# Kernel optimization log

Hardware: AMD Instinct MI355X
Metric: run time of the kernel (lower is better)

Reference implementation:

```python
import jax, jax.numpy as jnp
import numpy as np

B, L, D, H, M, DFF = 16, 2048, 512, 8, 64, 2048
E = D // H
KERNELS = (13, 25)
K = len(KERNELS)


def _moving_avg(x, k):
    # Autoformer-style moving average: replicate-pad (k-1)//2 at both ends, AvgPool1d stride 1.
    pad = (k - 1) // 2
    xp = jnp.concatenate([jnp.repeat(x[:, :1], pad, axis=1), x, jnp.repeat(x[:, -1:], pad, axis=1)], axis=1)
    cs = jnp.cumsum(xp, axis=1)
    cs = jnp.concatenate([jnp.zeros_like(cs[:, :1]), cs], axis=1)
    return (cs[:, k:] - cs[:, :-k]) / k  # [B, L, D] for odd k


def _decomp(x, w, b):
    # mixture-of-experts decomposition: softmax(Linear(1->K)(x)) weighted sum of K moving averages
    means = jnp.stack([_moving_avg(x, k) for k in KERNELS], axis=-1)  # [B,L,D,K]
    gate = jax.nn.softmax(x[..., None] * w + b, axis=-1)              # [B,L,D,K]
    mean = jnp.sum(means * gate, axis=-1)
    return x - mean


def _forward(x, Wq, bq, Wk, bk, Wv, bv, Wo, bo, four_wr, four_wi, conv1_w, conv2_w, dec1_w, dec1_b, dec2_w, dec2_b, mode_index):
    Bx, Lx, Dx = x.shape
    # q/k/v projections (FourierBlock only consumes q; k,v projected per AutoCorrelationLayer)
    q = x @ Wq.T + bq
    _ = x @ Wk.T + bk
    _ = x @ Wv.T + bv
    qh = q.reshape(Bx, Lx, H, E).transpose(0, 2, 3, 1)  # [B,H,E,L]
    x_ft = jnp.fft.rfft(qh, axis=-1)                     # [B,H,E,L//2+1]
    xsel = x_ft[..., mode_index]                         # [B,H,E,M] gather selected modes
    w = (four_wr + 1j * four_wi).astype(x_ft.dtype)      # [H,E,E,M]
    out = jnp.einsum('bhem,heom->bhom', xsel, w)         # per-mode complex channel mix
    out_ft = jnp.zeros((Bx, H, E, Lx // 2 + 1), x_ft.dtype).at[..., :M].set(out)
    y = jnp.fft.irfft(out_ft, n=Lx, axis=-1)             # [B,H,E,L]
    y = y.transpose(0, 3, 1, 2).reshape(Bx, Lx, Dx)      # mix=True: seq-major before merge
    u = x + (y @ Wo.T + bo)
    r1 = _decomp(u, dec1_w, dec1_b)
    ffn = jax.nn.gelu(r1 @ conv1_w.T, approximate=False) @ conv2_w.T  # 1x1 convs == pointwise linears
    return _decomp(r1 + ffn, dec2_w, dec2_b)


def setup_inputs() -> dict:
    key = jax.random.key(0)
    ks = jax.random.split(key, 16)
    s = 0.02
    rng = np.random.default_rng(0)
    mode_index = jnp.asarray(np.sort(rng.choice(L // 2, size=M, replace=False)).astype(np.int32))
    scale = 1.0 / (D * D)
    return {
        'x': jax.random.normal(ks[0], (B, L, D), jnp.float32),
        'Wq': s * jax.random.normal(ks[1], (D, D), jnp.float32),
        'bq': jnp.zeros((D,), jnp.float32),
        'Wk': s * jax.random.normal(ks[2], (D, D), jnp.float32),
        'bk': jnp.zeros((D,), jnp.float32),
        'Wv': s * jax.random.normal(ks[3], (D, D), jnp.float32),
        'bv': jnp.zeros((D,), jnp.float32),
        'Wo': s * jax.random.normal(ks[4], (D, D), jnp.float32),
        'bo': jnp.zeros((D,), jnp.float32),
        'four_wr': scale * jax.random.uniform(ks[5], (H, E, E, M), jnp.float32),
        'four_wi': scale * jax.random.uniform(ks[6], (H, E, E, M), jnp.float32),
        'conv1_w': s * jax.random.normal(ks[7], (DFF, D), jnp.float32),
        'conv2_w': s * jax.random.normal(ks[8], (D, DFF), jnp.float32),
        'dec1_w': 0.1 * jax.random.normal(ks[9], (K,), jnp.float32),
        'dec1_b': jnp.zeros((K,), jnp.float32),
        'dec2_w': 0.1 * jax.random.normal(ks[10], (K,), jnp.float32),
        'dec2_b': jnp.zeros((K,), jnp.float32),
        'mode_index': mode_index,
    }


def reference(x, Wq, bq, Wk, bk, Wv, bv, Wo, bo, four_wr, four_wi, conv1_w, conv2_w, dec1_w, dec1_b, dec2_w, dec2_b, mode_index):
    return _forward(x, Wq, bq, Wk, bk, Wv, bv, Wo, bo, four_wr, four_wi, conv1_w, conv2_w, dec1_w, dec1_b, dec2_w, dec2_b, mode_index)
```

## Files before the change

### kernel.cpp

```cpp
#include <hip/hip_runtime.h>
#include <math.h>


#define EPI_GELU   1
#define EPI_RES    2
#define EPI_SPLIT  3
#define EPI_WQFOLD 4
#define EPI_INVU   5

typedef __attribute__((ext_vector_type(8))) short short8;
typedef __attribute__((ext_vector_type(4))) float f32x4;

#define AS1 __attribute__((address_space(1)))
#define AS3 __attribute__((address_space(3)))

__device__ __forceinline__ void gll16(const void* g, void* l) {
    __builtin_amdgcn_global_load_lds((const AS1 void*)g, (AS3 void*)l, 16, 0, 0);
}

__device__ __forceinline__ float gelu_exact(float v) {
    return 0.5f * v * (1.0f + erff(v * 0.70710678118654752f));
}

__device__ __forceinline__ unsigned short f2bf(float f) {
    unsigned u = __builtin_bit_cast(unsigned, f);
    unsigned r = (u + 0x7fffu + ((u >> 16) & 1u)) >> 16;
    return (unsigned short)r;
}
__device__ __forceinline__ float bf2f(unsigned short h) {
    unsigned u = ((unsigned)h) << 16;
    return __builtin_bit_cast(float, u);
}

template<int BM, int BN, int EPI, bool ALO, bool BLO>
__global__ __launch_bounds__(512)
void gemm_hl(const unsigned short* __restrict__ Ah, const unsigned short* __restrict__ Al, long long sAb,
             const unsigned short* __restrict__ Bh, const unsigned short* __restrict__ Bl, long long sBb,
             float* __restrict__ Cf, unsigned short* __restrict__ Ch, unsigned short* __restrict__ Cl,
             long long sCb,
             const unsigned short* __restrict__ Rh, const unsigned short* __restrict__ Rl,
             const float* __restrict__ resf, long long sRb,
             const float* __restrict__ bias, const int* __restrict__ midx,
             int N, int K)
{
    constexpr int MI = BM / 32, NJ = BN / 64;
    __shared__ __align__(16) unsigned short sA[ALO ? 2 : 1][BM * 32];
    __shared__ __align__(16) unsigned short sB[BLO ? 2 : 1][BN * 32];

    const int tid = threadIdx.x, lane = tid & 63, wid = tid >> 6;
    const int wm = wid >> 2, wn = wid & 3;
    const int m0 = blockIdx.y * BM, n0 = blockIdx.x * BN;
    const int z = blockIdx.z;

    Ah += (size_t)z * sAb; if (ALO) Al += (size_t)z * sAb;
    Bh += (size_t)z * sBb; if (BLO) Bl += (size_t)z * sBb;

    f32x4 acc[MI][NJ] = {};

    const int srr = lane >> 2;
    const int sp  = lane & 3;

    for (int k0 = 0; k0 < K; k0 += 32) {
        for (int ch = wid; ch < BM / 16; ch += 8) {
            int row = ch * 16 + srr;
            int ls = sp ^ ((row >> 1) & 3);
            size_t g = (size_t)(m0 + row) * K + k0 + ls * 8;
            gll16(Ah + g, &sA[0][ch * 512]);
            if (ALO) gll16(Al + g, &sA[1][ch * 512]);
        }
        for (int ch = wid; ch < BN / 16; ch += 8) {
            int row = ch * 16 + srr;
            int ls = sp ^ ((row >> 1) & 3);
            size_t g = (size_t)(n0 + row) * K + k0 + ls * 8;
            gll16(Bh + g, &sB[0][ch * 512]);
            if (BLO) gll16(Bl + g, &sB[1][ch * 512]);
        }
        __syncthreads();

        short8 a[ALO ? 2 : 1][MI], b[BLO ? 2 : 1][NJ];
        const int s = lane >> 4;
#pragma unroll
        for (int i = 0; i < MI; ++i) {
            int r = wm * (BM / 2) + i * 16 + (lane & 15);
            int off = r * 32 + (s ^ ((r >> 1) & 3)) * 8;
            a[0][i] = *reinterpret_cast<const short8*>(&sA[0][off]);
            if (ALO) a[1][i] = *reinterpret_cast<const short8*>(&sA[1][off]);
        }
#pragma unroll
        for (int j = 0; j < NJ; ++j) {
            int r = wn * (BN / 4) + j * 16 + (lane & 15);
            int off = r * 32 + (s ^ ((r >> 1) & 3)) * 8;
            b[0][j] = *reinterpret_cast<const short8*>(&sB[0][off]);
            if (BLO) b[1][j] = *reinterpret_cast<const short8*>(&sB[1][off]);
        }
#pragma unroll
        for (int i = 0; i < MI; ++i)
#pragma unroll
            for (int j = 0; j < NJ; ++j) {
                acc[i][j] = __builtin_amdgcn_mfma_f32_16x16x32_bf16(a[0][i], b[0][j], acc[i][j], 0, 0, 0);
                if (BLO)
                    acc[i][j] = __builtin_amdgcn_mfma_f32_16x16x32_bf16(a[0][i], b[1][j], acc[i][j], 0, 0, 0);
                if (ALO)
                    acc[i][j] = __builtin_amdgcn_mfma_f32_16x16x32_bf16(a[1][i], b[0][j], acc[i][j], 0, 0, 0);
            }
        __syncthreads();
    }

    const int cr = (lane >> 4) * 4, cc = lane & 15;
#pragma unroll
    for (int i = 0; i < MI; ++i)
#pragma unroll
        for (int j = 0; j < NJ; ++j)
#pragma unroll
            for (int r = 0; r < 4; ++r) {
                int m = m0 + wm * (BM / 2) + i * 16 + cr + r;
                int n = n0 + wn * (BN / 4) + j * 16 + cc;
                size_t idx = (size_t)z * sCb + (size_t)m * N + n;
                float v = acc[i][j][r];
                if (EPI == EPI_GELU) {
                    Ch[idx] = f2bf(gelu_exact(v));
                } else if (EPI == EPI_RES) {
                    size_t ri = (size_t)m * N + n;
                    Cf[idx] = v + bf2f(Rh[ri]) + bf2f(Rl[ri]);
                } else if (EPI == EPI_SPLIT) {
                    unsigned short h = f2bf(v);
                    Ch[idx] = h;
                    Cl[idx] = f2bf(v - bf2f(h));
                } else if (EPI == EPI_WQFOLD) {
                    if (n < 64 && midx[n] == 0) v += bias[m] * 2048.0f;
                    Cf[idx] = v;
                } else if (EPI == EPI_INVU) {
                    size_t ri = (size_t)z * sRb + (size_t)m * N + n;
                    Cf[idx] = v + resf[ri] + bias[n];
                }
            }
}

__global__ __launch_bounds__(256)
void gemm_dft(const unsigned short* __restrict__ Ath, const unsigned short* __restrict__ Atl,
              const float* __restrict__ X, long long sXb,
              float* __restrict__ P)
{
    __shared__ __align__(16) unsigned short sA[2][64 * 32];
    __shared__ __align__(16) unsigned sB[2][64 * 20];

    const int tid = threadIdx.x, lane = tid & 63, wid = tid >> 6;
    const int wm = wid >> 1, wn = wid & 1;
    const int m0 = blockIdx.y * 64, n0 = blockIdx.x * 64;
    const int z = blockIdx.z;
    const int b = z >> 2, ks = z & 3;
    X += (size_t)b * sXb;

    f32x4 acc[2][2] = {};

    const int arow = wid * 16 + (lane >> 2);
    const int als  = (lane & 3) ^ ((arow >> 1) & 3);
    const int lp = tid >> 4;
    const int d4 = (tid & 15) * 4;

    for (int kk = 0; kk < 512; kk += 32) {
        const int k0 = ks * 512 + kk;
        size_t gA = (size_t)(m0 + arow) * 2048 + k0 + als * 8;
        gll16(Ath + gA, &sA[0][wid * 512]);
        gll16(Atl + gA, &sA[1][wid * 512]);

        const float* xr = &X[(size_t)(k0 + 2 * lp) * 512 + n0 + d4];
        float4 v0 = *reinterpret_cast<const float4*>(xr);
        float4 v1 = *reinterpret_cast<const float4*>(xr + 512);
        float a0[4] = {v0.x, v0.y, v0.z, v0.w};
        float a1[4] = {v1.x, v1.y, v1.z, v1.w};
#pragma unroll
        for (int i = 0; i < 4; ++i) {
            int row = d4 + i;
            int slot = lp ^ (((row >> 3) & 3) << 2);
            unsigned short h0 = f2bf(a0[i]), h1 = f2bf(a1[i]);
            sB[0][row * 20 + slot] = (unsigned)h0 | ((unsigned)h1 << 16);
            unsigned short l0 = f2bf(a0[i] - bf2f(h0)), l1 = f2bf(a1[i] - bf2f(h1));
            sB[1][row * 20 + slot] = (unsigned)l0 | ((unsigned)l1 << 16);
        }
        __syncthreads();

        short8 a[2][2], b2[2][2];
        const int s = lane >> 4;
#pragma unroll
        for (int i = 0; i < 2; ++i) {
            int r = wm * 32 + i * 16 + (lane & 15);
            int off = r * 32 + (s ^ ((r >> 1) & 3)) * 8;
            a[0][i] = *reinterpret_cast<const short8*>(&sA[0][off]);
            a[1][i] = *reinterpret_cast<const short8*>(&sA[1][off]);
        }
#pragma unroll
        for (int j = 0; j < 2; ++j) {
            int d = wn * 32 + j * 16 + (lane & 15);
            int off = d * 20 + ((s * 4) ^ (((d >> 3) & 3) << 2));
            b2[0][j] = *reinterpret_cast<const short8*>(&sB[0][off]);
            b2[1][j] = *reinterpret_cast<const short8*>(&sB[1][off]);
        }
#pragma unroll
        for (int i = 0; i < 2; ++i)
#pragma unroll
            for (int j = 0; j < 2; ++j) {
                acc[i][j] = __builtin_amdgcn_mfma_f32_16x16x32_bf16(a[0][i], b2[0][j], acc[i][j], 0, 0, 0);
                acc[i][j] = __builtin_amdgcn_mfma_f32_16x16x32_bf16(a[0][i], b2[1][j], acc[i][j], 0, 0, 0);
                acc[i][j] = __builtin_amdgcn_mfma_f32_16x16x32_bf16(a[1][i], b2[0][j], acc[i][j], 0, 0, 0);
            }
        __syncthreads();
    }

    const int cr = (lane >> 4) * 4, cc = lane & 15;
#pragma unroll
    for (int i = 0; i < 2; ++i)
#pragma unroll
        for (int j = 0; j < 2; ++j)
#pragma unroll
            for (int r = 0; r < 4; ++r) {
                int m = m0 + wm * 32 + i * 16 + cr + r;
                int n = n0 + wn * 32 + j * 16 + cc;
                P[((size_t)z * 128 + m) * 512 + n] = acc[i][j][r];
            }
}

__global__ __launch_bounds__(256)
void dft_reduce(const float* __restrict__ P, unsigned short* __restrict__ Oh,
                unsigned short* __restrict__ Ol)
{
    int i = blockIdx.x * 256 + threadIdx.x;
    int b = i >> 14;
    int r = i & 16383;
    const float4* p = reinterpret_cast<const float4*>(P) + ((size_t)b * 4) * 16384 + r;
    float4 v = p[0];
    float4 v1 = p[16384], v2 = p[2 * 16384], v3 = p[3 * 16384];
    v.x += v1.x + v2.x + v3.x;
    v.y += v1.y + v2.y + v3.y;
    v.z += v1.z + v2.z + v3.z;
    v.w += v1.w + v2.w + v3.w;
    ushort4 h, l;
    h.x = f2bf(v.x); l.x = f2bf(v.x - bf2f(h.x));
    h.y = f2bf(v.y); l.y = f2bf(v.y - bf2f(h.y));
    h.z = f2bf(v.z); l.z = f2bf(v.z - bf2f(h.z));
    h.w = f2bf(v.w); l.w = f2bf(v.w - bf2f(h.w));
    size_t o = (size_t)b * 16384 + r;
    reinterpret_cast<ushort4*>(Oh)[o] = h;
    reinterpret_cast<ushort4*>(Ol)[o] = l;
}

__global__ __launch_bounds__(256)
void split_f32_kernel(const float* __restrict__ src, unsigned short* __restrict__ hi,
                      unsigned short* __restrict__ lo, int n4)
{
    int i = blockIdx.x * 256 + threadIdx.x;
    if (i >= n4) return;
    float4 v = reinterpret_cast<const float4*>(src)[i];
    ushort4 h, l;
    h.x = f2bf(v.x); l.x = f2bf(v.x - bf2f(h.x));
    h.y = f2bf(v.y); l.y = f2bf(v.y - bf2f(h.y));
    h.z = f2bf(v.z); l.z = f2bf(v.z - bf2f(h.z));
    h.w = f2bf(v.w); l.w = f2bf(v.w - bf2f(h.w));
    reinterpret_cast<ushort4*>(hi)[i] = h;
    reinterpret_cast<ushort4*>(lo)[i] = l;
}

__global__ void build_tables_kernel(const int* __restrict__ midx,
                                    unsigned short* __restrict__ fth, unsigned short* __restrict__ ftl,
                                    unsigned short* __restrict__ ith, unsigned short* __restrict__ itl)
{
    const int l = blockIdx.x;
    const int t = threadIdx.x;
    const int m = t & 63;
    const bool im = t >= 64;
    const float c0 = 6.28318530717958647692f / 2048.0f;

    int f = midx[m];
    int ph = (f * l) & 2047;
    float s, c;
    sincosf(c0 * (float)ph, &s, &c);
    float v = im ? -s : c;
    unsigned short h = f2bf(v);
    fth[(size_t)t * 2048 + l] = h;
    ftl[(size_t)t * 2048 + l] = f2bf(v - bf2f(h));

    int ph2 = (m * l) & 2047;
    float s2, c2;
    sincosf(c0 * (float)ph2, &s2, &c2);
    float v2 = im ? s2 : c2;
    unsigned short h2 = f2bf(v2);
    ith[(size_t)l * 128 + t] = h2;
    itl[(size_t)l * 128 + t] = f2bf(v2 - bf2f(h2));
}

__global__ __launch_bounds__(256)
void mode_mix_kernel(const float* __restrict__ xsel,
                     const float* __restrict__ wr, const float* __restrict__ wi,
                     unsigned short* __restrict__ cth, unsigned short* __restrict__ ctl)
{
    const int m = blockIdx.x;
    const int h = blockIdx.y;
    const int tid = threadIdx.x;

    __shared__ float xr[16][64], xi[16][64];
    __shared__ float wrs[64][65], wis[64][65];

    for (int i = tid; i < 4096; i += 256) {
        int e = i >> 6, o = i & 63;
        size_t g = (((size_t)h * 64 + e) * 64 + o) * 64 + m;
        wrs[e][o] = wr[g];
        wis[e][o] = wi[g];
    }
    for (int i = tid; i < 1024; i += 256) {
        int bb = i >> 6, e = i & 63;
        size_t g = ((size_t)bb * 512 + h * 64 + e) * 128;
        xr[bb][e] = xsel[g + m];
        xi[bb][e] = xsel[g + 64 + m];
    }
    __syncthreads();

    const int o = tid & 63;
    const int bq4 = tid >> 6;
    const float sc_r = (m == 0) ? (1.0f / 2048.0f) : (2.0f / 2048.0f);
    const float sc_i = (m == 0) ? 0.0f : (-2.0f / 2048.0f);

    for (int q = 0; q < 4; ++q) {
        int bb = bq4 * 4 + q;
        float or_ = 0.f, oi_ = 0.f;
#pragma unroll 16
        for (int e = 0; e < 64; ++e) {
            float xrv = xr[bb][e], xiv = xi[bb][e];
            float wrv = wrs[e][o], wiv = wis[e][o];
            or_ += xrv * wrv - xiv * wiv;
            oi_ += xrv * wiv + xiv * wrv;
        }
        size_t base = ((size_t)bb * 128 + m) * 512 + (size_t)h * 64 + o;
        float vr = or_ * sc_r;
        unsigned short hr = f2bf(vr);
        cth[base] = hr; ctl[base] = f2bf(vr - bf2f(hr));
        float vi = oi_ * sc_i;
        unsigned short hi2 = f2bf(vi);
        cth[base + 64 * 512] = hi2; ctl[base + 64 * 512] = f2bf(vi - bf2f(hi2));
    }
}

template<bool SPLIT>
__global__ __launch_bounds__(256)
void decomp_kernel(const float* __restrict__ X, float* __restrict__ Rf,
                   unsigned short* __restrict__ Rh, unsigned short* __restrict__ Rl,
                   const float* __restrict__ w, const float* __restrict__ bg)
{
    const int d = blockIdx.x * 256 + threadIdx.x;
    const int l0 = blockIdx.y * 64;
    const int b = blockIdx.z;
    const float w0 = w[0], w1 = w[1], b0 = bg[0], b1 = bg[1];

    const float* Xp = X + (size_t)b * 2048 * 512 + d;
    const size_t obase = (size_t)b * 2048 * 512 + d;

    float s1 = 0.f, s2 = 0.f;
    for (int i = l0 - 12; i <= l0 + 12; ++i) {
        int ic = min(max(i, 0), 2047);
        float v = Xp[(size_t)ic * 512];
        s2 += v;
        if (i >= l0 - 6 && i <= l0 + 6) s1 += v;
    }
    for (int l = l0; l < l0 + 64; ++l) {
        float xv = Xp[(size_t)l * 512];
        float m1 = s1 * (1.0f / 13.0f);
        float m2 = s2 * (1.0f / 25.0f);
        float e0 = xv * w0 + b0, e1 = xv * w1 + b1;
        float mx = fmaxf(e0, e1);
        float g0 = expf(e0 - mx), g1 = expf(e1 - mx);
        float mean = (g0 * m1 + g1 * m2) / (g0 + g1);
        float rv = xv - mean;
        size_t oi = obase + (size_t)l * 512;
        if (SPLIT) {
            unsigned short h = f2bf(rv);
            Rh[oi] = h;
            Rl[oi] = f2bf(rv - bf2f(h));
        } else {
            Rf[oi] = rv;
        }
        s1 += Xp[(size_t)min(l + 7, 2047) * 512] - Xp[(size_t)max(l - 6, 0) * 512];
        s2 += Xp[(size_t)min(l + 13, 2047) * 512] - Xp[(size_t)max(l - 12, 0) * 512];
    }
}

extern "C" void kernel_launch(void* const* d_in, const int* in_sizes, int n_in,
                              void* d_out, int out_size, void* d_ws, size_t ws_size,
                              hipStream_t stream)
{
    const float* x    = (const float*)d_in[0];
    const float* Wq   = (const float*)d_in[1];
    const float* bq   = (const float*)d_in[2];
    const float* Wo   = (const float*)d_in[7];
    const float* bo   = (const float*)d_in[8];
    const float* fwr  = (const float*)d_in[9];
    const float* fwi  = (const float*)d_in[10];
    const float* c1w  = (const float*)d_in[11];
    const float* c2w  = (const float*)d_in[12];
    const float* d1w  = (const float*)d_in[13];
    const float* d1b  = (const float*)d_in[14];
    const float* d2w  = (const float*)d_in[15];
    const float* d2b  = (const float*)d_in[16];
    const int*   midx = (const int*)d_in[17];
    float* out = (float*)d_out;
    float* ws  = (float*)d_ws;

    float* region0 = ws;
    unsigned short* p1 = (unsigned short*)(ws + 16777216);
    unsigned short* fth = p1;
    unsigned short* ftl = p1 + 262144;
    unsigned short* ith = p1 + 2 * 262144;
    unsigned short* itl = p1 + 3 * 262144;
    unsigned short* wqh = p1 + 4 * 262144;
    unsigned short* wql = p1 + 5 * 262144;
    unsigned short* woh = p1 + 6 * 262144;
    unsigned short* wol = p1 + 7 * 262144;
    unsigned short* xfh = p1 + 2097152;
    unsigned short* xfl = p1 + 3145728;
    unsigned short* cth = p1 + 4194304;
    unsigned short* ctl = p1 + 5242880;
    unsigned short* zth = p1 + 6291456;
    unsigned short* ztl = p1 + 7340288;
    float* xsel = (float*)(p1 + 8388608);

    unsigned short* c1h = p1;
    unsigned short* c1l = p1 + 1048576;
    unsigned short* c2h = p1 + 2 * 1048576;
    unsigned short* c2l = p1 + 3 * 1048576;
    unsigned short* hh  = (unsigned short*)(ws + 18874368);
    const size_t hbase = 72ull << 20;
    const int R = (ws_size >= hbase + (size_t)8192 * 2048 * 2) ? 8192 : 4096;

    unsigned short* r1h = (unsigned short*)d_out;
    unsigned short* r1l = r1h + 16777216;

    const long long sBL = (long long)2048 * 512;
    const long long sP  = 65536;

    build_tables_kernel<<<2048, 128, 0, stream>>>(midx, fth, ftl, ith, itl);
    split_f32_kernel<<<256, 256, 0, stream>>>(Wq, wqh, wql, 65536);
    split_f32_kernel<<<256, 256, 0, stream>>>(Wo, woh, wol, 65536);

    gemm_dft<<<dim3(8, 2, 64), 256, 0, stream>>>(fth, ftl, x, sBL, region0);
    dft_reduce<<<1024, 256, 0, stream>>>(region0, xfh, xfl);

    gemm_hl<64, 64, EPI_WQFOLD, true, true><<<dim3(2, 8, 16), 512, 0, stream>>>(
        wqh, wql, 0, xfh, xfl, sP, xsel, nullptr, nullptr, sP,
        nullptr, nullptr, nullptr, 0, bq, midx, 128, 512);

    mode_mix_kernel<<<dim3(64, 8), 256, 0, stream>>>(xsel, fwr, fwi, cth, ctl);

    gemm_hl<64, 64, EPI_SPLIT, true, true><<<dim3(2, 8, 16), 512, 0, stream>>>(
        woh, wol, 0, cth, ctl, sP, nullptr, zth, ztl, sP,
        nullptr, nullptr, nullptr, 0, nullptr, nullptr, 128, 512);

    gemm_hl<128, 64, EPI_INVU, true, true><<<dim3(8, 16, 16), 512, 0, stream>>>(
        ith, itl, 0, zth, ztl, sP, region0, nullptr, nullptr, sBL,
        nullptr, nullptr, x, sBL, bo, nullptr, 512, 128);

    decomp_kernel<true><<<dim3(2, 32, 16), 256, 0, stream>>>(
        region0, nullptr, r1h, r1l, d1w, d1b);

    split_f32_kernel<<<1024, 256, 0, stream>>>(c1w, c1h, c1l, 262144);
    split_f32_kernel<<<1024, 256, 0, stream>>>(c2w, c2h, c2l, 262144);

    const int nc = 32768 / R;
    for (int c = 0; c < nc; ++c) {
        const unsigned short* r1hc = r1h + (size_t)c * R * 512;
        const unsigned short* r1lc = r1l + (size_t)c * R * 512;
        gemm_hl<128, 128, EPI_GELU, true, true><<<dim3(16, R / 128), 512, 0, stream>>>(
            r1hc, r1lc, 0, c1h, c1l, 0, nullptr, hh, nullptr, 0,
            nullptr, nullptr, nullptr, 0, nullptr, nullptr, 2048, 512);
        gemm_hl<128, 64, EPI_RES, false, true><<<dim3(8, R / 128), 512, 0, stream>>>(
            hh, nullptr, 0, c2h, c2l, 0, region0 + (size_t)c * R * 512, nullptr, nullptr, 0,
            r1hc, r1lc, nullptr, 0, nullptr, nullptr, 512, 2048);
    }

    decomp_kernel<false><<<dim3(2, 32, 16), 256, 0, stream>>>(
        region0, out, nullptr, nullptr, d2w, d2b);
}
```

Before: 840.3 us.

## Drop hi/lo bf16 split, use single bf16 GEMMs with XCD-aware block swizzle

```diff
diff --git a/kernel.cpp b/kernel.cpp
--- a/kernel.cpp
+++ b/kernel.cpp
@@ -4,7 +4,7 @@
 
 #define EPI_GELU   1
 #define EPI_RES    2
-#define EPI_SPLIT  3
+#define EPI_BF16   3
 #define EPI_WQFOLD 4
 #define EPI_INVU   5
 
@@ -32,28 +32,35 @@
     return __builtin_bit_cast(float, u);
 }
 
-template<int BM, int BN, int EPI, bool ALO, bool BLO>
+template<int BM, int BN, int EPI>
 __global__ __launch_bounds__(512)
-void gemm_hl(const unsigned short* __restrict__ Ah, const unsigned short* __restrict__ Al, long long sAb,
-             const unsigned short* __restrict__ Bh, const unsigned short* __restrict__ Bl, long long sBb,
-             float* __restrict__ Cf, unsigned short* __restrict__ Ch, unsigned short* __restrict__ Cl,
-             long long sCb,
+void gemm_hl(const unsigned short* __restrict__ Ah, long long sAb,
+             const unsigned short* __restrict__ Bh, long long sBb,
+             float* __restrict__ Cf, unsigned short* __restrict__ Ch, long long sCb,
              const unsigned short* __restrict__ Rh, const unsigned short* __restrict__ Rl,
              const float* __restrict__ resf, long long sRb,
              const float* __restrict__ bias, const int* __restrict__ midx,
              int N, int K)
 {
     constexpr int MI = BM / 32, NJ = BN / 64;
-    __shared__ __align__(16) unsigned short sA[ALO ? 2 : 1][BM * 32];
-    __shared__ __align__(16) unsigned short sB[BLO ? 2 : 1][BN * 32];
+    __shared__ __align__(16) unsigned short sA[BM * 32];
+    __shared__ __align__(16) unsigned short sB[BN * 32];
 
     const int tid = threadIdx.x, lane = tid & 63, wid = tid >> 6;
     const int wm = wid >> 2, wn = wid & 3;
-    const int m0 = blockIdx.y * BM, n0 = blockIdx.x * BN;
+
+    const int gx = gridDim.x;
+    int flat = blockIdx.y * gx + blockIdx.x;
+    const int nwg = gx * gridDim.y;
+    if ((nwg & 7) == 0) {
+        const int cpx = nwg >> 3;
+        flat = (flat & 7) * cpx + (flat >> 3);
+    }
+    const int m0 = (flat / gx) * BM, n0 = (flat % gx) * BN;
     const int z = blockIdx.z;
 
-    Ah += (size_t)z * sAb; if (ALO) Al += (size_t)z * sAb;
-    Bh += (size_t)z * sBb; if (BLO) Bl += (size_t)z * sBb;
+    Ah += (size_t)z * sAb;
+    Bh += (size_t)z * sBb;
 
     f32x4 acc[MI][NJ] = {};
 
@@ -64,45 +71,32 @@
         for (int ch = wid; ch < BM / 16; ch += 8) {
             int row = ch * 16 + srr;
             int ls = sp ^ ((row >> 1) & 3);
-            size_t g = (size_t)(m0 + row) * K + k0 + ls * 8;
-            gll16(Ah + g, &sA[0][ch * 512]);
-            if (ALO) gll16(Al + g, &sA[1][ch * 512]);
+            gll16(Ah + (size_t)(m0 + row) * K + k0 + ls * 8, &sA[ch * 512]);
         }
         for (int ch = wid; ch < BN / 16; ch += 8) {
             int row = ch * 16 + srr;
             int ls = sp ^ ((row >> 1) & 3);
-            size_t g = (size_t)(n0 + row) * K + k0 + ls * 8;
-            gll16(Bh + g, &sB[0][ch * 512]);
-            if (BLO) gll16(Bl + g, &sB[1][ch * 512]);
+            gll16(Bh + (size_t)(n0 + row) * K + k0 + ls * 8, &sB[ch * 512]);
         }
         __syncthreads();
 
-        short8 a[ALO ? 2 : 1][MI], b[BLO ? 2 : 1][NJ];
+        short8 a[MI], b[NJ];
         const int s = lane >> 4;
 #pragma unroll
         for (int i = 0; i < MI; ++i) {
             int r = wm * (BM / 2) + i * 16 + (lane & 15);
-            int off = r * 32 + (s ^ ((r >> 1) & 3)) * 8;
-            a[0][i] = *reinterpret_cast<const short8*>(&sA[0][off]);
-            if (ALO) a[1][i] = *reinterpret_cast<const short8*>(&sA[1][off]);
+            a[i] = *reinterpret_cast<const short8*>(&sA[r * 32 + (s ^ ((r >> 1) & 3)) * 8]);
         }
 #pragma unroll
         for (int j = 0; j < NJ; ++j) {
             int r = wn * (BN / 4) + j * 16 + (lane & 15);
-            int off = r * 32 + (s ^ ((r >> 1) & 3)) * 8;
-            b[0][j] = *reinterpret_cast<const short8*>(&sB[0][off]);
-            if (BLO) b[1][j] = *reinterpret_cast<const short8*>(&sB[1][off]);
+            b[j] = *reinterpret_cast<const short8*>(&sB[r * 32 + (s ^ ((r >> 1) & 3)) * 8]);
         }
 #pragma unroll
         for (int i = 0; i < MI; ++i)
 #pragma unroll
-            for (int j = 0; j < NJ; ++j) {
-                acc[i][j] = __builtin_amdgcn_mfma_f32_16x16x32_bf16(a[0][i], b[0][j], acc[i][j], 0, 0, 0);
-                if (BLO)
-                    acc[i][j] = __builtin_amdgcn_mfma_f32_16x16x32_bf16(a[0][i], b[1][j], acc[i][j], 0, 0, 0);
-                if (ALO)
-                    acc[i][j] = __builtin_amdgcn_mfma_f32_16x16x32_bf16(a[1][i], b[0][j], acc[i][j], 0, 0, 0);
-            }
+            for (int j = 0; j < NJ; ++j)
+                acc[i][j] = __builtin_amdgcn_mfma_f32_16x16x32_bf16(a[i], b[j], acc[i][j], 0, 0, 0);
         __syncthreads();
     }
 
@@ -122,10 +116,8 @@
                 } else if (EPI == EPI_RES) {
                     size_t ri = (size_t)m * N + n;
                     Cf[idx] = v + bf2f(Rh[ri]) + bf2f(Rl[ri]);
-                } else if (EPI == EPI_SPLIT) {
-                    unsigned short h = f2bf(v);
-                    Ch[idx] = h;
-                    Cl[idx] = f2bf(v - bf2f(h));
+                } else if (EPI == EPI_BF16) {
+                    Ch[idx] = f2bf(v);
                 } else if (EPI == EPI_WQFOLD) {
                     if (n < 64 && midx[n] == 0) v += bias[m] * 2048.0f;
                     Cf[idx] = v;
@@ -137,12 +129,12 @@
 }
 
 __global__ __launch_bounds__(256)
-void gemm_dft(const unsigned short* __restrict__ Ath, const unsigned short* __restrict__ Atl,
+void gemm_dft(const unsigned short* __restrict__ Ath,
               const float* __restrict__ X, long long sXb,
               float* __restrict__ P)
 {
-    __shared__ __align__(16) unsigned short sA[2][64 * 32];
-    __shared__ __align__(16) unsigned sB[2][64 * 20];
+    __shared__ __align__(16) unsigned short sA[64 * 32];
+    __shared__ __align__(16) unsigned sB[64 * 20];
 
     const int tid = threadIdx.x, lane = tid & 63, wid = tid >> 6;
     const int wm = wid >> 1, wn = wid & 1;
@@ -160,9 +152,7 @@
 
     for (int kk = 0; kk < 512; kk += 32) {
         const int k0 = ks * 512 + kk;
-        size_t gA = (size_t)(m0 + arow) * 2048 + k0 + als * 8;
-        gll16(Ath + gA, &sA[0][wid * 512]);
-        gll16(Atl + gA, &sA[1][wid * 512]);
+        gll16(Ath + (size_t)(m0 + arow) * 2048 + k0 + als * 8, &sA[wid * 512]);
 
         const float* xr = &X[(size_t)(k0 + 2 * lp) * 512 + n0 + d4];
         float4 v0 = *reinterpret_cast<const float4*>(xr);
@@ -173,37 +163,28 @@
         for (int i = 0; i < 4; ++i) {
             int row = d4 + i;
             int slot = lp ^ (((row >> 3) & 3) << 2);
-            unsigned short h0 = f2bf(a0[i]), h1 = f2bf(a1[i]);
-            sB[0][row * 20 + slot] = (unsigned)h0 | ((unsigned)h1 << 16);
-            unsigned short l0 = f2bf(a0[i] - bf2f(h0)), l1 = f2bf(a1[i] - bf2f(h1));
-            sB[1][row * 20 + slot] = (unsigned)l0 | ((unsigned)l1 << 16);
+            sB[row * 20 + slot] = (unsigned)f2bf(a0[i]) | ((unsigned)f2bf(a1[i]) << 16);
         }
         __syncthreads();
 
-        short8 a[2][2], b2[2][2];
+        short8 a[2], b2[2];
         const int s = lane >> 4;
 #pragma unroll
         for (int i = 0; i < 2; ++i) {
             int r = wm * 32 + i * 16 + (lane & 15);
-            int off = r * 32 + (s ^ ((r >> 1) & 3)) * 8;
-            a[0][i] = *reinterpret_cast<const short8*>(&sA[0][off]);
-            a[1][i] = *reinterpret_cast<const short8*>(&sA[1][off]);
+            a[i] = *reinterpret_cast<const short8*>(&sA[r * 32 + (s ^ ((r >> 1) & 3)) * 8]);
         }
 #pragma unroll
         for (int j = 0; j < 2; ++j) {
             int d = wn * 32 + j * 16 + (lane & 15);
             int off = d * 20 + ((s * 4) ^ (((d >> 3) & 3) << 2));
-            b2[0][j] = *reinterpret_cast<const short8*>(&sB[0][off]);
-            b2[1][j] = *reinterpret_cast<const short8*>(&sB[1][off]);
+            b2[j] = *reinterpret_cast<const short8*>(&sB[off]);
         }
 #pragma unroll
         for (int i = 0; i < 2; ++i)
 #pragma unroll
-            for (int j = 0; j < 2; ++j) {
-                acc[i][j] = __builtin_amdgcn_mfma_f32_16x16x32_bf16(a[0][i], b2[0][j], acc[i][j], 0, 0, 0);
-                acc[i][j] = __builtin_amdgcn_mfma_f32_16x16x32_bf16(a[0][i], b2[1][j], acc[i][j], 0, 0, 0);
-                acc[i][j] = __builtin_amdgcn_mfma_f32_16x16x32_bf16(a[1][i], b2[0][j], acc[i][j], 0, 0, 0);
-            }
+            for (int j = 0; j < 2; ++j)
+                acc[i][j] = __builtin_amdgcn_mfma_f32_16x16x32_bf16(a[i], b2[j], acc[i][j], 0, 0, 0);
         __syncthreads();
     }
 
@@ -221,8 +202,7 @@
 }
 
 __global__ __launch_bounds__(256)
-void dft_reduce(const float* __restrict__ P, unsigned short* __restrict__ Oh,
-                unsigned short* __restrict__ Ol)
+void dft_reduce(const float* __restrict__ P, unsigned short* __restrict__ Oh)
 {
     int i = blockIdx.x * 256 + threadIdx.x;
     int b = i >> 14;
@@ -234,35 +214,25 @@
     v.y += v1.y + v2.y + v3.y;
     v.z += v1.z + v2.z + v3.z;
     v.w += v1.w + v2.w + v3.w;
-    ushort4 h, l;
-    h.x = f2bf(v.x); l.x = f2bf(v.x - bf2f(h.x));
-    h.y = f2bf(v.y); l.y = f2bf(v.y - bf2f(h.y));
-    h.z = f2bf(v.z); l.z = f2bf(v.z - bf2f(h.z));
-    h.w = f2bf(v.w); l.w = f2bf(v.w - bf2f(h.w));
-    size_t o = (size_t)b * 16384 + r;
-    reinterpret_cast<ushort4*>(Oh)[o] = h;
-    reinterpret_cast<ushort4*>(Ol)[o] = l;
+    ushort4 h;
+    h.x = f2bf(v.x); h.y = f2bf(v.y); h.z = f2bf(v.z); h.w = f2bf(v.w);
+    reinterpret_cast<ushort4*>(Oh)[(size_t)b * 16384 + r] = h;
 }
 
 __global__ __launch_bounds__(256)
-void split_f32_kernel(const float* __restrict__ src, unsigned short* __restrict__ hi,
-                      unsigned short* __restrict__ lo, int n4)
+void cvt_bf16_kernel(const float* __restrict__ src, unsigned short* __restrict__ hi, int n4)
 {
     int i = blockIdx.x * 256 + threadIdx.x;
     if (i >= n4) return;
     float4 v = reinterpret_cast<const float4*>(src)[i];
-    ushort4 h, l;
-    h.x = f2bf(v.x); l.x = f2bf(v.x - bf2f(h.x));
-    h.y = f2bf(v.y); l.y = f2bf(v.y - bf2f(h.y));
-    h.z = f2bf(v.z); l.z = f2bf(v.z - bf2f(h.z));
-    h.w = f2bf(v.w); l.w = f2bf(v.w - bf2f(h.w));
+    ushort4 h;
+    h.x = f2bf(v.x); h.y = f2bf(v.y); h.z = f2bf(v.z); h.w = f2bf(v.w);
     reinterpret_cast<ushort4*>(hi)[i] = h;
-    reinterpret_cast<ushort4*>(lo)[i] = l;
 }
 
 __global__ void build_tables_kernel(const int* __restrict__ midx,
-                                    unsigned short* __restrict__ fth, unsigned short* __restrict__ ftl,
-                                    unsigned short* __restrict__ ith, unsigned short* __restrict__ itl)
+                                    unsigned short* __restrict__ fth,
+                                    unsigned short* __restrict__ ith)
 {
     const int l = blockIdx.x;
     const int t = threadIdx.x;
@@ -274,24 +244,18 @@
     int ph = (f * l) & 2047;
     float s, c;
     sincosf(c0 * (float)ph, &s, &c);
-    float v = im ? -s : c;
-    unsigned short h = f2bf(v);
-    fth[(size_t)t * 2048 + l] = h;
-    ftl[(size_t)t * 2048 + l] = f2bf(v - bf2f(h));
+    fth[(size_t)t * 2048 + l] = f2bf(im ? -s : c);
 
     int ph2 = (m * l) & 2047;
     float s2, c2;
     sincosf(c0 * (float)ph2, &s2, &c2);
-    float v2 = im ? s2 : c2;
-    unsigned short h2 = f2bf(v2);
-    ith[(size_t)l * 128 + t] = h2;
-    itl[(size_t)l * 128 + t] = f2bf(v2 - bf2f(h2));
+    ith[(size_t)l * 128 + t] = f2bf(im ? s2 : c2);
 }
 
 __global__ __launch_bounds__(256)
 void mode_mix_kernel(const float* __restrict__ xsel,
                      const float* __restrict__ wr, const float* __restrict__ wi,
-                     unsigned short* __restrict__ cth, unsigned short* __restrict__ ctl)
+                     unsigned short* __restrict__ cth)
 {
     const int m = blockIdx.x;
     const int h = blockIdx.y;
@@ -330,12 +294,8 @@
             oi_ += xrv * wiv + xiv * wrv;
         }
         size_t base = ((size_t)bb * 128 + m) * 512 + (size_t)h * 64 + o;
-        float vr = or_ * sc_r;
-        unsigned short hr = f2bf(vr);
-        cth[base] = hr; ctl[base] = f2bf(vr - bf2f(hr));
-        float vi = oi_ * sc_i;
-        unsigned short hi2 = f2bf(vi);
-        cth[base + 64 * 512] = hi2; ctl[base + 64 * 512] = f2bf(vi - bf2f(hi2));
+        cth[base] = f2bf(or_ * sc_r);
+        cth[base + 64 * 512] = f2bf(oi_ * sc_i);
     }
 }
 
@@ -346,7 +306,7 @@
                    const float* __restrict__ w, const float* __restrict__ bg)
 {
     const int d = blockIdx.x * 256 + threadIdx.x;
-    const int l0 = blockIdx.y * 64;
+    const int l0 = blockIdx.y * 32;
     const int b = blockIdx.z;
     const float w0 = w[0], w1 = w[1], b0 = bg[0], b1 = bg[1];
 
@@ -360,7 +320,7 @@
         s2 += v;
         if (i >= l0 - 6 && i <= l0 + 6) s1 += v;
     }
-    for (int l = l0; l < l0 + 64; ++l) {
+    for (int l = l0; l < l0 + 32; ++l) {
         float xv = Xp[(size_t)l * 512];
         float m1 = s1 * (1.0f / 13.0f);
         float m2 = s2 * (1.0f / 25.0f);
@@ -406,25 +366,16 @@
     float* region0 = ws;
     unsigned short* p1 = (unsigned short*)(ws + 16777216);
     unsigned short* fth = p1;
-    unsigned short* ftl = p1 + 262144;
-    unsigned short* ith = p1 + 2 * 262144;
-    unsigned short* itl = p1 + 3 * 262144;
-    unsigned short* wqh = p1 + 4 * 262144;
-    unsigned short* wql = p1 + 5 * 262144;
-    unsigned short* woh = p1 + 6 * 262144;
-    unsigned short* wol = p1 + 7 * 262144;
-    unsigned short* xfh = p1 + 2097152;
-    unsigned short* xfl = p1 + 3145728;
-    unsigned short* cth = p1 + 4194304;
-    unsigned short* ctl = p1 + 5242880;
-    unsigned short* zth = p1 + 6291456;
-    unsigned short* ztl = p1 + 7340288;
-    float* xsel = (float*)(p1 + 8388608);
+    unsigned short* ith = p1 + 262144;
+    unsigned short* wqh = p1 + 2 * 262144;
+    unsigned short* woh = p1 + 3 * 262144;
+    unsigned short* xfh = p1 + 1048576;
+    unsigned short* cth = p1 + 2097152;
+    unsigned short* zth = p1 + 3145728;
+    float* xsel = (float*)(p1 + 4194304);
 
     unsigned short* c1h = p1;
-    unsigned short* c1l = p1 + 1048576;
-    unsigned short* c2h = p1 + 2 * 1048576;
-    unsigned short* c2l = p1 + 3 * 1048576;
+    unsigned short* c2h = p1 + 1048576;
     unsigned short* hh  = (unsigned short*)(ws + 18874368);
     const size_t hbase = 72ull << 20;
     const int R = (ws_size >= hbase + (size_t)8192 * 2048 * 2) ? 8192 : 4096;
@@ -435,45 +386,45 @@
     const long long sBL = (long long)2048 * 512;
     const long long sP  = 65536;
 
-    build_tables_kernel<<<2048, 128, 0, stream>>>(midx, fth, ftl, ith, itl);
-    split_f32_kernel<<<256, 256, 0, stream>>>(Wq, wqh, wql, 65536);
-    split_f32_kernel<<<256, 256, 0, stream>>>(Wo, woh, wol, 65536);
-
-    gemm_dft<<<dim3(8, 2, 64), 256, 0, stream>>>(fth, ftl, x, sBL, region0);
-    dft_reduce<<<1024, 256, 0, stream>>>(region0, xfh, xfl);
-
-    gemm_hl<64, 64, EPI_WQFOLD, true, true><<<dim3(2, 8, 16), 512, 0, stream>>>(
-        wqh, wql, 0, xfh, xfl, sP, xsel, nullptr, nullptr, sP,
+    build_tables_kernel<<<2048, 128, 0, stream>>>(midx, fth, ith);
+    cvt_bf16_kernel<<<256, 256, 0, stream>>>(Wq, wqh, 65536);
+    cvt_bf16_kernel<<<256, 256, 0, stream>>>(Wo, woh, 65536);
+
+    gemm_dft<<<dim3(8, 2, 64), 256, 0, stream>>>(fth, x, sBL, region0);
+    dft_reduce<<<1024, 256, 0, stream>>>(region0, xfh);
+
+    gemm_hl<64, 64, EPI_WQFOLD><<<dim3(2, 8, 16), 512, 0, stream>>>(
+        wqh, 0, xfh, sP, xsel, nullptr, sP,
         nullptr, nullptr, nullptr, 0, bq, midx, 128, 512);
 
-    mode_mix_kernel<<<dim3(64, 8), 256, 0, stream>>>(xsel, fwr, fwi, cth, ctl);
-
-    gemm_hl<64, 64, EPI_SPLIT, true, true><<<dim3(2, 8, 16), 512, 0, stream>>>(
-        woh, wol, 0, cth, ctl, sP, nullptr, zth, ztl, sP,
+    mode_mix_kernel<<<dim3(64, 8), 256, 0, stream>>>(xsel, fwr, fwi, cth);
+
+    gemm_hl<64, 64, EPI_BF16><<<dim3(2, 8, 16), 512, 0, stream>>>(
+        woh, 0, cth, sP, nullptr, zth, sP,
         nullptr, nullptr, nullptr, 0, nullptr, nullptr, 128, 512);
 
-    gemm_hl<128, 64, EPI_INVU, true, true><<<dim3(8, 16, 16), 512, 0, stream>>>(
-        ith, itl, 0, zth, ztl, sP, region0, nullptr, nullptr, sBL,
+    gemm_hl<128, 128, EPI_INVU><<<dim3(4, 16, 16), 512, 0, stream>>>(
+        ith, 0, zth, sP, region0, nullptr, sBL,
         nullptr, nullptr, x, sBL, bo, nullptr, 512, 128);
 
-    decomp_kernel<true><<<dim3(2, 32, 16), 256, 0, stream>>>(
+    decomp_kernel<true><<<dim3(2, 64, 16), 256, 0, stream>>>(
         region0, nullptr, r1h, r1l, d1w, d1b);
 
-    split_f32_kernel<<<1024, 256, 0, stream>>>(c1w, c1h, c1l, 262144);
-    split_f32_kernel<<<1024, 256, 0, stream>>>(c2w, c2h, c2l, 262144);
+    cvt_bf16_kernel<<<1024, 256, 0, stream>>>(c1w, c1h, 262144);
+    cvt_bf16_kernel<<<1024, 256, 0, stream>>>(c2w, c2h, 262144);
 
     const int nc = 32768 / R;
     for (int c = 0; c < nc; ++c) {
         const unsigned short* r1hc = r1h + (size_t)c * R * 512;
         const unsigned short* r1lc = r1l + (size_t)c * R * 512;
-        gemm_hl<128, 128, EPI_GELU, true, true><<<dim3(16, R / 128), 512, 0, stream>>>(
-            r1hc, r1lc, 0, c1h, c1l, 0, nullptr, hh, nullptr, 0,
+        gemm_hl<128, 128, EPI_GELU><<<dim3(16, R / 128), 512, 0, stream>>>(
+            r1hc, 0, c1h, 0, nullptr, hh, 0,
             nullptr, nullptr, nullptr, 0, nullptr, nullptr, 2048, 512);
-        gemm_hl<128, 64, EPI_RES, false, true><<<dim3(8, R / 128), 512, 0, stream>>>(
-            hh, nullptr, 0, c2h, c2l, 0, region0 + (size_t)c * R * 512, nullptr, nullptr, 0,
+        gemm_hl<128, 128, EPI_RES><<<dim3(4, R / 128), 512, 0, stream>>>(
+            hh, 0, c2h, 0, region0 + (size_t)c * R * 512, nullptr, 0,
             r1hc, r1lc, nullptr, 0, nullptr, nullptr, 512, 2048);
     }
 
-    decomp_kernel<false><<<dim3(2, 32, 16), 256, 0, stream>>>(
+    decomp_kernel<false><<<dim3(2, 64, 16), 256, 0, stream>>>(
         region0, out, nullptr, nullptr, d2w, d2b);
 }
```

After: 674.3 us. -19.8%, faster.
